# Kernel optimization log

Hardware: AMD Instinct MI355X
Metric: run time of the kernel (lower is better)

The kernel has to match this reference:

```python
import jax, jax.numpy as jnp
import numpy as np

N, D = 8192, 128
WEIGHT = 0.01


def _neg_flat_indices(n):
    # Replicates: mask = ones(n,n); fill_diagonal_(0); mask[i,i+1]=0; mask[i+1,i]=0
    # i.e. keep (i,j) with j != i, j != i+1, j != i-1. Row-major flatnonzero
    # reproduces torch's sim[mask] flattening order exactly.
    i = np.arange(n)[:, None]
    j = np.arange(n)[None, :]
    mask = (j != i) & (j != i + 1) & (j != i - 1)
    idx = np.flatnonzero(mask)
    assert idx.size == (n - 1) * (n - 2)
    return idx


NEG_IDX = jnp.asarray(_neg_flat_indices(N))  # [(N-1)*(N-2)] int32/int64 constant


def setup_inputs() -> dict:
    key = jax.random.key(0)
    factor = jax.random.normal(key, (N, D), dtype=jnp.float32)
    return {"factor": factor}


def reference(factor):
    n = factor.shape[0]
    # F.normalize(factor): L2-normalize rows with eps=1e-12
    norms = jnp.linalg.norm(factor, axis=1, keepdims=True)
    f = factor / jnp.maximum(norms, 1e-12)
    sim = f @ f.T                                   # [N, N] gram matrix
    pos = jnp.diagonal(sim, offset=1).reshape(n - 1, 1)      # [N-1, 1]
    neg = sim.reshape(-1)[NEG_IDX].reshape(n - 1, n - 2)     # [N-1, N-2]
    logits = jnp.concatenate([pos, neg], axis=1)             # [N-1, N-1]
    # CrossEntropyLoss(reduction='sum') with all-zero labels:
    # sum_i (logsumexp(logits_i) - logits_i[0])
    loss = jnp.sum(jax.nn.logsumexp(logits, axis=1) - logits[:, 0])
    loss = loss / n
    return -WEIGHT * loss
```

## Files before the change

### kernel.cpp

```cpp
#include <hip/hip_runtime.h>
#include <hip/hip_bf16.h>

#define N 8192
#define D 128
#define WEIGHT 0.01f
#define NTILES 64
#define NBLK 2080

typedef __bf16 bf16x8 __attribute__((ext_vector_type(8)));
typedef float floatx4 __attribute__((ext_vector_type(4)));

__global__ __launch_bounds__(256) void k_norm(const float* __restrict__ x,
                                              __hip_bfloat16* __restrict__ fb) {
    int gid = blockIdx.x * 256 + threadIdx.x;
    int row = gid >> 4;
    int c   = gid & 15;
    const float4* xr = (const float4*)(x + (size_t)row * D + c * 8);
    float4 f0 = xr[0], f1 = xr[1];
    float s = f0.x * f0.x + f0.y * f0.y + f0.z * f0.z + f0.w * f0.w
            + f1.x * f1.x + f1.y * f1.y + f1.z * f1.z + f1.w * f1.w;
    s += __shfl_xor(s, 1, 64);
    s += __shfl_xor(s, 2, 64);
    s += __shfl_xor(s, 4, 64);
    s += __shfl_xor(s, 8, 64);
    float inv = 1.0f / fmaxf(sqrtf(s), 1e-12f);
    union { __hip_bfloat16 h[8]; uint4 u; } pk;
    pk.h[0] = __float2bfloat16(f0.x * inv);
    pk.h[1] = __float2bfloat16(f0.y * inv);
    pk.h[2] = __float2bfloat16(f0.z * inv);
    pk.h[3] = __float2bfloat16(f0.w * inv);
    pk.h[4] = __float2bfloat16(f1.x * inv);
    pk.h[5] = __float2bfloat16(f1.y * inv);
    pk.h[6] = __float2bfloat16(f1.z * inv);
    pk.h[7] = __float2bfloat16(f1.w * inv);
    ((uint4*)fb)[(size_t)row * 16 + (c ^ (row & 15))] = pk.u;
}

__global__ __launch_bounds__(256, 2) void k_gram(const __hip_bfloat16* __restrict__ fb,
                                                 float* __restrict__ Prow,
                                                 float* __restrict__ Pcol,
                                                 float* __restrict__ p,
                                                 float* __restrict__ ep) {
    int b = blockIdx.x;
    int bi = (int)((2.0 * NTILES + 1.0 - sqrt((2.0 * NTILES + 1.0) * (2.0 * NTILES + 1.0) - 8.0 * (double)b)) * 0.5);
    while (bi * NTILES - bi * (bi - 1) / 2 > b) --bi;
    while ((bi + 1) * NTILES - (bi + 1) * bi / 2 <= b) ++bi;
    int bj = bi + (b - (bi * NTILES - bi * (bi - 1) / 2));

    __shared__ uint4 Ab[128 * 16];
    __shared__ uint4 Bb[128 * 16];
    __shared__ float PR[2][128];
    __shared__ float PC[2][128];

    const int t = threadIdx.x;
    const int lane = t & 63;
    const int wid  = t >> 6;
    const int wrow = wid >> 1, wcol = wid & 1;
    const int col0 = lane & 15;
    const int quad = lane >> 4;
    const int rbase = bi * 128, cbase = bj * 128;

    const uint4* gA = (const uint4*)fb + (size_t)rbase * 16;
    const uint4* gB = (const uint4*)fb + (size_t)cbase * 16;
    #pragma unroll
    for (int i = 0; i < 8; ++i) {
        int ca = wid * 512 + i * 64;
        __builtin_amdgcn_global_load_lds(
            (const __attribute__((address_space(1))) void*)(gA + ca + lane),
            (__attribute__((address_space(3))) void*)&Ab[ca], 16, 0, 0);
        __builtin_amdgcn_global_load_lds(
            (const __attribute__((address_space(1))) void*)(gB + ca + lane),
            (__attribute__((address_space(3))) void*)&Bb[ca], 16, 0, 0);
    }
    __syncthreads();

    floatx4 acc[4][4];
    #pragma unroll
    for (int a = 0; a < 4; ++a)
        #pragma unroll
        for (int c = 0; c < 4; ++c)
            acc[a][c] = (floatx4){0.0f, 0.0f, 0.0f, 0.0f};

    #pragma unroll
    for (int ks = 0; ks < 4; ++ks) {
        bf16x8 af[4], bfr[4];
        int j = ks * 4 + quad;
        int jsw = j ^ col0;
        #pragma unroll
        for (int mt = 0; mt < 4; ++mt) {
            int rl = wrow * 64 + mt * 16 + col0;
            af[mt] = *(const bf16x8*)&Ab[rl * 16 + jsw];
        }
        #pragma unroll
        for (int nt = 0; nt < 4; ++nt) {
            int cl = wcol * 64 + nt * 16 + col0;
            bfr[nt] = *(const bf16x8*)&Bb[cl * 16 + jsw];
        }
        #pragma unroll
        for (int mt = 0; mt < 4; ++mt)
            #pragma unroll
            for (int nt = 0; nt < 4; ++nt)
                acc[mt][nt] = __builtin_amdgcn_mfma_f32_16x16x32_bf16(af[mt], bfr[nt], acc[mt][nt], 0, 0, 0);
    }

    float v[16];
    float colpart[4];
    #pragma unroll
    for (int m = 0; m < 16; ++m) v[m] = 0.0f;
    #pragma unroll
    for (int m = 0; m < 4; ++m) colpart[m] = 0.0f;

    if (bj > bi + 1) {
        #pragma unroll
        for (int mt = 0; mt < 4; ++mt)
            #pragma unroll
            for (int nt = 0; nt < 4; ++nt)
                #pragma unroll
                for (int reg = 0; reg < 4; ++reg) {
                    float e = __expf(acc[mt][nt][reg]);
                    v[mt * 4 + reg] += e;
                    colpart[nt] += e;
                }
    } else {
        #pragma unroll
        for (int mt = 0; mt < 4; ++mt)
            #pragma unroll
            for (int nt = 0; nt < 4; ++nt)
                #pragma unroll
                for (int reg = 0; reg < 4; ++reg) {
                    int r = rbase + wrow * 64 + mt * 16 + quad * 4 + reg;
                    int c = cbase + wcol * 64 + nt * 16 + col0;
                    float s0 = acc[mt][nt][reg];
                    float e = __expf(s0);
                    if (c == r + 1) { p[r] = s0; ep[r] = e; }
                    e = (c > r) ? e : 0.0f;
                    v[mt * 4 + reg] += e;
                    colpart[nt] += e;
                }
    }

    float v8[8];
    #pragma unroll
    for (int k = 0; k < 8; ++k) {
        float a = v[2 * k], bb = v[2 * k + 1];
        float give = (lane & 1) ? a : bb;
        float keep = (lane & 1) ? bb : a;
        v8[k] = keep + __shfl_xor(give, 1, 64);
    }
    float v4[4];
    #pragma unroll
    for (int k = 0; k < 4; ++k) {
        float a = v8[2 * k], bb = v8[2 * k + 1];
        float give = (lane & 2) ? a : bb;
        float keep = (lane & 2) ? bb : a;
        v4[k] = keep + __shfl_xor(give, 2, 64);
    }
    float v2[2];
    #pragma unroll
    for (int k = 0; k < 2; ++k) {
        float a = v4[2 * k], bb = v4[2 * k + 1];
        float give = (lane & 4) ? a : bb;
        float keep = (lane & 4) ? bb : a;
        v2[k] = keep + __shfl_xor(give, 4, 64);
    }
    {
        float a = v2[0], bb = v2[1];
        float give = (lane & 8) ? a : bb;
        float keep = (lane & 8) ? bb : a;
        float v1 = keep + __shfl_xor(give, 8, 64);
        int rowl = wrow * 64 + (col0 >> 2) * 16 + quad * 4 + (col0 & 3);
        PR[wcol][rowl] = v1;
    }
    {
        float c2[2];
        #pragma unroll
        for (int k = 0; k < 2; ++k) {
            float a = colpart[2 * k];
            float bb = colpart[2 * k + 1];
            float give = (lane & 16) ? a : bb;
            float keep = (lane & 16) ? bb : a;
            c2[k] = keep + __shfl_xor(give, 16, 64);
        }
        float a = c2[0], bb = c2[1];
        float give = (lane & 32) ? a : bb;
        float keep = (lane & 32) ? bb : a;
        float cv = keep + __shfl_xor(give, 32, 64);
        PC[wrow][wcol * 64 + lane] = cv;
    }
    __syncthreads();

    if (t < 128) {
        Prow[(size_t)b * 128 + t] = PR[0][t] + PR[1][t];
    } else {
        int c = t - 128;
        Pcol[(size_t)b * 128 + c] = PC[0][c] + PC[1][c];
    }
}

__global__ __launch_bounds__(256) void k_reduce(const float* __restrict__ Prow,
                                                const float* __restrict__ Pcol,
                                                float* __restrict__ U,
                                                float* __restrict__ L) {
    int tile = blockIdx.x;
    int tid = threadIdx.x;
    int base_t = tile * NTILES - tile * (tile - 1) / 2;
    if (tid < 128) {
        float s = 0.0f;
        for (int bj = tile; bj < NTILES; ++bj)
            s += Prow[(size_t)(base_t + bj - tile) * 128 + tid];
        U[tile * 128 + tid] = s;
    } else {
        int c = tid - 128;
        float s = 0.0f;
        for (int bi = 0; bi <= tile; ++bi) {
            int bb = bi * NTILES - bi * (bi - 1) / 2 + (tile - bi);
            s += Pcol[(size_t)bb * 128 + c];
        }
        L[tile * 128 + c] = s;
    }
}

__global__ __launch_bounds__(1024) void k_final(const float* __restrict__ U,
                                                const float* __restrict__ L,
                                                const float* __restrict__ p,
                                                const float* __restrict__ ep,
                                                float* __restrict__ out) {
    __shared__ float swred[16];
    float s = 0.0f;
    for (int i = threadIdx.x; i < N - 1; i += 1024) {
        float tt = U[i] + L[i + 1] - ep[i];
        s += __logf(tt) - p[i];
    }
    #pragma unroll
    for (int m = 1; m < 64; m <<= 1) s += __shfl_xor(s, m, 64);
    int lane = threadIdx.x & 63, wid = threadIdx.x >> 6;
    if (lane == 0) swred[wid] = s;
    __syncthreads();
    if (threadIdx.x == 0) {
        float tot = 0.0f;
        #pragma unroll
        for (int w = 0; w < 16; ++w) tot += swred[w];
        out[0] = -WEIGHT * tot / (float)N;
    }
}

extern "C" void kernel_launch(void* const* d_in, const int* in_sizes, int n_in,
                              void* d_out, int out_size, void* d_ws, size_t ws_size,
                              hipStream_t stream) {
    const float* x = (const float*)d_in[0];
    float* out = (float*)d_out;
    char* ws = (char*)d_ws;
    __hip_bfloat16* fb = (__hip_bfloat16*)ws;
    float* p    = (float*)(ws + (size_t)N * D * 2);
    float* ep   = p + N;
    float* U    = ep + N;
    float* L    = U + N;
    float* Prow = L + N;
    float* Pcol = Prow + (size_t)NBLK * 128;

    hipLaunchKernelGGL(k_norm,   dim3(512),  dim3(256),  0, stream, x, fb);
    hipLaunchKernelGGL(k_gram,   dim3(NBLK), dim3(256),  0, stream, fb, Prow, Pcol, p, ep);
    hipLaunchKernelGGL(k_reduce, dim3(64),   dim3(256),  0, stream, Prow, Pcol, U, L);
    hipLaunchKernelGGL(k_final,  dim3(1),    dim3(1024), 0, stream, U, L, p, ep, out);
}
```

Before: 96.93 us.

## Process four column tiles per block with double-buffered B prefetch

Each k_gram block now handles up to four consecutive column tiles of the same row tile, launching 544 blocks instead of 2080. The A tile is loaded once and reused, while the next B tile is prefetched into a second LDS buffer during the current tile's MFMA and exp work. Partial-sum writeback is deferred by one iteration through double-buffered PR/PC arrays. The intent is to cut redundant A loads and per-block launch and prologue cost. In exchange, launch bounds drop to one block per CU, so occupancy falls and per-row work is uneven because the last chunk of each row has fewer tiles.

```diff
diff --git a/kernel.cpp b/kernel.cpp
--- a/kernel.cpp
+++ b/kernel.cpp
@@ -6,6 +6,8 @@
 #define WEIGHT 0.01f
 #define NTILES 64
 #define NBLK 2080
+#define TPB 4
+#define GRID 544
 
 typedef __bf16 bf16x8 __attribute__((ext_vector_type(8)));
 typedef float floatx4 __attribute__((ext_vector_type(4)));
@@ -36,21 +38,25 @@
     ((uint4*)fb)[(size_t)row * 16 + (c ^ (row & 15))] = pk.u;
 }
 
-__global__ __launch_bounds__(256, 2) void k_gram(const __hip_bfloat16* __restrict__ fb,
+__global__ __launch_bounds__(256, 1) void k_gram(const __hip_bfloat16* __restrict__ fb,
                                                  float* __restrict__ Prow,
                                                  float* __restrict__ Pcol,
                                                  float* __restrict__ p,
                                                  float* __restrict__ ep) {
     int b = blockIdx.x;
-    int bi = (int)((2.0 * NTILES + 1.0 - sqrt((2.0 * NTILES + 1.0) * (2.0 * NTILES + 1.0) - 8.0 * (double)b)) * 0.5);
-    while (bi * NTILES - bi * (bi - 1) / 2 > b) --bi;
-    while ((bi + 1) * NTILES - (bi + 1) * bi / 2 <= b) ++bi;
-    int bj = bi + (b - (bi * NTILES - bi * (bi - 1) / 2));
-
-    __shared__ uint4 Ab[128 * 16];
-    __shared__ uint4 Bb[128 * 16];
-    __shared__ float PR[2][128];
-    __shared__ float PC[2][128];
+    int bi = 0;
+    for (; bi < NTILES; ++bi) {
+        int cnt = (NTILES - bi + TPB - 1) >> 2;
+        if (b < cnt) break;
+        b -= cnt;
+    }
+    int bj0 = bi + b * TPB;
+    int ntile = min(TPB, NTILES - bj0);
+
+    __shared__ uint4 Ab[2048];
+    __shared__ uint4 Bb[2][2048];
+    __shared__ float PR[2][2][128];
+    __shared__ float PC[2][2][128];
 
     const int t = threadIdx.x;
     const int lane = t & 63;
@@ -58,142 +64,181 @@
     const int wrow = wid >> 1, wcol = wid & 1;
     const int col0 = lane & 15;
     const int quad = lane >> 4;
-    const int rbase = bi * 128, cbase = bj * 128;
-
-    const uint4* gA = (const uint4*)fb + (size_t)rbase * 16;
-    const uint4* gB = (const uint4*)fb + (size_t)cbase * 16;
-    #pragma unroll
-    for (int i = 0; i < 8; ++i) {
-        int ca = wid * 512 + i * 64;
-        __builtin_amdgcn_global_load_lds(
-            (const __attribute__((address_space(1))) void*)(gA + ca + lane),
-            (__attribute__((address_space(3))) void*)&Ab[ca], 16, 0, 0);
-        __builtin_amdgcn_global_load_lds(
-            (const __attribute__((address_space(1))) void*)(gB + ca + lane),
-            (__attribute__((address_space(3))) void*)&Bb[ca], 16, 0, 0);
-    }
+    const int rbase = bi * 128;
+    const int tri0 = bi * NTILES - bi * (bi - 1) / 2;
+
+    const uint4* gf = (const uint4*)fb;
+
+    {
+        const uint4* gA = gf + (size_t)rbase * 16;
+        const uint4* gB = gf + (size_t)(bj0 * 128) * 16;
+        #pragma unroll
+        for (int i = 0; i < 8; ++i) {
+            int ca = wid * 512 + i * 64;
+            __builtin_amdgcn_global_load_lds(
+                (const __attribute__((address_space(1))) void*)(gA + ca + lane),
+                (__attribute__((address_space(3))) void*)&Ab[ca], 16, 0, 0);
+            __builtin_amdgcn_global_load_lds(
+                (const __attribute__((address_space(1))) void*)(gB + ca + lane),
+                (__attribute__((address_space(3))) void*)&Bb[0][ca], 16, 0, 0);
+        }
+    }
+
+    for (int tt = 0; tt < ntile; ++tt) {
+        const int cur = tt & 1;
+        const int bjt = bj0 + tt;
+        const int cbase = bjt * 128;
+        const int tgid = tri0 + (bjt - bi);
+
+        __syncthreads();
+
+        if (tt + 1 < ntile) {
+            const uint4* gBn = gf + (size_t)((bjt + 1) * 128) * 16;
+            #pragma unroll
+            for (int i = 0; i < 8; ++i) {
+                int ca = wid * 512 + i * 64;
+                __builtin_amdgcn_global_load_lds(
+                    (const __attribute__((address_space(1))) void*)(gBn + ca + lane),
+                    (__attribute__((address_space(3))) void*)&Bb[cur ^ 1][ca], 16, 0, 0);
+            }
+        }
+
+        if (tt > 0) {
+            int pprev = (tt - 1) & 1;
+            int tprev = tgid - 1;
+            if (t < 128) {
+                Prow[(size_t)tprev * 128 + t] = PR[pprev][0][t] + PR[pprev][1][t];
+            } else {
+                int c = t - 128;
+                Pcol[(size_t)tprev * 128 + c] = PC[pprev][0][c] + PC[pprev][1][c];
+            }
+        }
+
+        floatx4 acc[4][4];
+        #pragma unroll
+        for (int a = 0; a < 4; ++a)
+            #pragma unroll
+            for (int c = 0; c < 4; ++c)
+                acc[a][c] = (floatx4){0.0f, 0.0f, 0.0f, 0.0f};
+
+        #pragma unroll
+        for (int ks = 0; ks < 4; ++ks) {
+            bf16x8 af[4], bfr[4];
+            int j = ks * 4 + quad;
+            int jsw = j ^ col0;
+            #pragma unroll
+            for (int mt = 0; mt < 4; ++mt) {
+                int rl = wrow * 64 + mt * 16 + col0;
+                af[mt] = *(const bf16x8*)&Ab[rl * 16 + jsw];
+            }
+            #pragma unroll
+            for (int nt = 0; nt < 4; ++nt) {
+                int cl = wcol * 64 + nt * 16 + col0;
+                bfr[nt] = *(const bf16x8*)&Bb[cur][cl * 16 + jsw];
+            }
+            #pragma unroll
+            for (int mt = 0; mt < 4; ++mt)
+                #pragma unroll
+                for (int nt = 0; nt < 4; ++nt)
+                    acc[mt][nt] = __builtin_amdgcn_mfma_f32_16x16x32_bf16(af[mt], bfr[nt], acc[mt][nt], 0, 0, 0);
+        }
+
+        float v[16];
+        float colpart[4];
+        #pragma unroll
+        for (int m = 0; m < 16; ++m) v[m] = 0.0f;
+        #pragma unroll
+        for (int m = 0; m < 4; ++m) colpart[m] = 0.0f;
+
+        if (bjt > bi + 1) {
+            #pragma unroll
+            for (int mt = 0; mt < 4; ++mt)
+                #pragma unroll
+                for (int nt = 0; nt < 4; ++nt)
+                    #pragma unroll
+                    for (int reg = 0; reg < 4; ++reg) {
+                        float e = __expf(acc[mt][nt][reg]);
+                        v[mt * 4 + reg] += e;
+                        colpart[nt] += e;
+                    }
+        } else {
+            #pragma unroll
+            for (int mt = 0; mt < 4; ++mt)
+                #pragma unroll
+                for (int nt = 0; nt < 4; ++nt)
+                    #pragma unroll
+                    for (int reg = 0; reg < 4; ++reg) {
+                        int r = rbase + wrow * 64 + mt * 16 + quad * 4 + reg;
+                        int c = cbase + wcol * 64 + nt * 16 + col0;
+                        float s0 = acc[mt][nt][reg];
+                        float e = __expf(s0);
+                        if (c == r + 1) { p[r] = s0; ep[r] = e; }
+                        e = (c > r) ? e : 0.0f;
+                        v[mt * 4 + reg] += e;
+                        colpart[nt] += e;
+                    }
+        }
+
+        float v8[8];
+        #pragma unroll
+        for (int k = 0; k < 8; ++k) {
+            float a = v[2 * k], bb = v[2 * k + 1];
+            float give = (lane & 1) ? a : bb;
+            float keep = (lane & 1) ? bb : a;
+            v8[k] = keep + __shfl_xor(give, 1, 64);
+        }
+        float v4[4];
+        #pragma unroll
+        for (int k = 0; k < 4; ++k) {
+            float a = v8[2 * k], bb = v8[2 * k + 1];
+            float give = (lane & 2) ? a : bb;
+            float keep = (lane & 2) ? bb : a;
+            v4[k] = keep + __shfl_xor(give, 2, 64);
+        }
+        float v2[2];
+        #pragma unroll
+        for (int k = 0; k < 2; ++k) {
+            float a = v4[2 * k], bb = v4[2 * k + 1];
+            float give = (lane & 4) ? a : bb;
+            float keep = (lane & 4) ? bb : a;
+            v2[k] = keep + __shfl_xor(give, 4, 64);
+        }
+        {
+            float a = v2[0], bb = v2[1];
+            float give = (lane & 8) ? a : bb;
+            float keep = (lane & 8) ? bb : a;
+            float v1 = keep + __shfl_xor(give, 8, 64);
+            int rowl = wrow * 64 + (col0 >> 2) * 16 + quad * 4 + (col0 & 3);
+            PR[cur][wcol][rowl] = v1;
+        }
+        {
+            float c2[2];
+            #pragma unroll
+            for (int k = 0; k < 2; ++k) {
+                float a = colpart[2 * k];
+                float bb = colpart[2 * k + 1];
+                float give = (lane & 16) ? a : bb;
+                float keep = (lane & 16) ? bb : a;
+                c2[k] = keep + __shfl_xor(give, 16, 64);
+            }
+            float a = c2[0], bb = c2[1];
+            float give = (lane & 32) ? a : bb;
+            float keep = (lane & 32) ? bb : a;
+            float cv = keep + __shfl_xor(give, 32, 64);
+            PC[cur][wrow][wcol * 64 + lane] = cv;
+        }
+    }
+
     __syncthreads();
-
-    floatx4 acc[4][4];
-    #pragma unroll
-    for (int a = 0; a < 4; ++a)
-        #pragma unroll
-        for (int c = 0; c < 4; ++c)
-            acc[a][c] = (floatx4){0.0f, 0.0f, 0.0f, 0.0f};
-
-    #pragma unroll
-    for (int ks = 0; ks < 4; ++ks) {
-        bf16x8 af[4], bfr[4];
-        int j = ks * 4 + quad;
-        int jsw = j ^ col0;
-        #pragma unroll
-        for (int mt = 0; mt < 4; ++mt) {
-            int rl = wrow * 64 + mt * 16 + col0;
-            af[mt] = *(const bf16x8*)&Ab[rl * 16 + jsw];
-        }
-        #pragma unroll
-        for (int nt = 0; nt < 4; ++nt) {
-            int cl = wcol * 64 + nt * 16 + col0;
-            bfr[nt] = *(const bf16x8*)&Bb[cl * 16 + jsw];
-        }
-        #pragma unroll
-        for (int mt = 0; mt < 4; ++mt)
-            #pragma unroll
-            for (int nt = 0; nt < 4; ++nt)
-                acc[mt][nt] = __builtin_amdgcn_mfma_f32_16x16x32_bf16(af[mt], bfr[nt], acc[mt][nt], 0, 0, 0);
-    }
-
-    float v[16];
-    float colpart[4];
-    #pragma unroll
-    for (int m = 0; m < 16; ++m) v[m] = 0.0f;
-    #pragma unroll
-    for (int m = 0; m < 4; ++m) colpart[m] = 0.0f;
-
-    if (bj > bi + 1) {
-        #pragma unroll
-        for (int mt = 0; mt < 4; ++mt)
-            #pragma unroll
-            for (int nt = 0; nt < 4; ++nt)
-                #pragma unroll
-                for (int reg = 0; reg < 4; ++reg) {
-                    float e = __expf(acc[mt][nt][reg]);
-                    v[mt * 4 + reg] += e;
-                    colpart[nt] += e;
-                }
-    } else {
-        #pragma unroll
-        for (int mt = 0; mt < 4; ++mt)
-            #pragma unroll
-            for (int nt = 0; nt < 4; ++nt)
-                #pragma unroll
-                for (int reg = 0; reg < 4; ++reg) {
-                    int r = rbase + wrow * 64 + mt * 16 + quad * 4 + reg;
-                    int c = cbase + wcol * 64 + nt * 16 + col0;
-                    float s0 = acc[mt][nt][reg];
-                    float e = __expf(s0);
-                    if (c == r + 1) { p[r] = s0; ep[r] = e; }
-                    e = (c > r) ? e : 0.0f;
-                    v[mt * 4 + reg] += e;
-                    colpart[nt] += e;
-                }
-    }
-
-    float v8[8];
-    #pragma unroll
-    for (int k = 0; k < 8; ++k) {
-        float a = v[2 * k], bb = v[2 * k + 1];
-        float give = (lane & 1) ? a : bb;
-        float keep = (lane & 1) ? bb : a;
-        v8[k] = keep + __shfl_xor(give, 1, 64);
-    }
-    float v4[4];
-    #pragma unroll
-    for (int k = 0; k < 4; ++k) {
-        float a = v8[2 * k], bb = v8[2 * k + 1];
-        float give = (lane & 2) ? a : bb;
-        float keep = (lane & 2) ? bb : a;
-        v4[k] = keep + __shfl_xor(give, 2, 64);
-    }
-    float v2[2];
-    #pragma unroll
-    for (int k = 0; k < 2; ++k) {
-        float a = v4[2 * k], bb = v4[2 * k + 1];
-        float give = (lane & 4) ? a : bb;
-        float keep = (lane & 4) ? bb : a;
-        v2[k] = keep + __shfl_xor(give, 4, 64);
-    }
     {
-        float a = v2[0], bb = v2[1];
-        float give = (lane & 8) ? a : bb;
-        float keep = (lane & 8) ? bb : a;
-        float v1 = keep + __shfl_xor(give, 8, 64);
-        int rowl = wrow * 64 + (col0 >> 2) * 16 + quad * 4 + (col0 & 3);
-        PR[wcol][rowl] = v1;
-    }
-    {
-        float c2[2];
-        #pragma unroll
-        for (int k = 0; k < 2; ++k) {
-            float a = colpart[2 * k];
-            float bb = colpart[2 * k + 1];
-            float give = (lane & 16) ? a : bb;
-            float keep = (lane & 16) ? bb : a;
-            c2[k] = keep + __shfl_xor(give, 16, 64);
-        }
-        float a = c2[0], bb = c2[1];
-        float give = (lane & 32) ? a : bb;
-        float keep = (lane & 32) ? bb : a;
-        float cv = keep + __shfl_xor(give, 32, 64);
-        PC[wrow][wcol * 64 + lane] = cv;
-    }
-    __syncthreads();
-
-    if (t < 128) {
-        Prow[(size_t)b * 128 + t] = PR[0][t] + PR[1][t];
-    } else {
-        int c = t - 128;
-        Pcol[(size_t)b * 128 + c] = PC[0][c] + PC[1][c];
+        int pprev = (ntile - 1) & 1;
+        int tprev = tri0 + (bj0 + ntile - 1 - bi);
+        if (t < 128) {
+            Prow[(size_t)tprev * 128 + t] = PR[pprev][0][t] + PR[pprev][1][t];
+        } else {
+            int c = t - 128;
+            Pcol[(size_t)tprev * 128 + c] = PC[pprev][0][c] + PC[pprev][1][c];
+        }
     }
 }
 
@@ -259,7 +304,7 @@
     float* Pcol = Prow + (size_t)NBLK * 128;
 
     hipLaunchKernelGGL(k_norm,   dim3(512),  dim3(256),  0, stream, x, fb);
-    hipLaunchKernelGGL(k_gram,   dim3(NBLK), dim3(256),  0, stream, fb, Prow, Pcol, p, ep);
+    hipLaunchKernelGGL(k_gram,   dim3(GRID), dim3(256),  0, stream, fb, Prow, Pcol, p, ep);
     hipLaunchKernelGGL(k_reduce, dim3(64),   dim3(256),  0, stream, Prow, Pcol, U, L);
     hipLaunchKernelGGL(k_final,  dim3(1),    dim3(1024), 0, stream, U, L, p, ep, out);
 }
```

Result: slower. 109.2 us (+12.6%).

## Enlarge gram tiles to 256x256 with 512-thread blocks

Applied to the files above, without the earlier changes.

Doubles the upper-triangle gram tile from 128 to 256 rows and columns and uses 8 waves per block, each wave computing a 64x128 output slab. This cuts the block count from 2080 to 528, halves the per-element partial-sum traffic, and shrinks the reduction kernel to 32 tiles. The aim is better reuse of each loaded operand and less partial-sum writing and reduction overhead. In exchange, LDS use rises to about 128KB per block, which likely limits occupancy to one block per CU. The much smaller grid also risks poor load balance across CUs.

```diff
diff --git a/kernel.cpp b/kernel.cpp
--- a/kernel.cpp
+++ b/kernel.cpp
@@ -4,8 +4,8 @@
 #define N 8192
 #define D 128
 #define WEIGHT 0.01f
-#define NTILES 64
-#define NBLK 2080
+#define NT2 32
+#define NBLK2 528
 
 typedef __bf16 bf16x8 __attribute__((ext_vector_type(8)));
 typedef float floatx4 __attribute__((ext_vector_type(4)));
@@ -36,29 +36,28 @@
     ((uint4*)fb)[(size_t)row * 16 + (c ^ (row & 15))] = pk.u;
 }
 
-__global__ __launch_bounds__(256, 2) void k_gram(const __hip_bfloat16* __restrict__ fb,
+__global__ __launch_bounds__(512, 2) void k_gram(const __hip_bfloat16* __restrict__ fb,
                                                  float* __restrict__ Prow,
                                                  float* __restrict__ Pcol,
                                                  float* __restrict__ p,
                                                  float* __restrict__ ep) {
     int b = blockIdx.x;
-    int bi = (int)((2.0 * NTILES + 1.0 - sqrt((2.0 * NTILES + 1.0) * (2.0 * NTILES + 1.0) - 8.0 * (double)b)) * 0.5);
-    while (bi * NTILES - bi * (bi - 1) / 2 > b) --bi;
-    while ((bi + 1) * NTILES - (bi + 1) * bi / 2 <= b) ++bi;
-    int bj = bi + (b - (bi * NTILES - bi * (bi - 1) / 2));
-
-    __shared__ uint4 Ab[128 * 16];
-    __shared__ uint4 Bb[128 * 16];
-    __shared__ float PR[2][128];
-    __shared__ float PC[2][128];
+    int bi = 0;
+    while ((bi + 1) * NT2 - (bi + 1) * bi / 2 <= b) ++bi;
+    int bj = bi + (b - (bi * NT2 - bi * (bi - 1) / 2));
+
+    __shared__ uint4 Ab[4096];
+    __shared__ uint4 Bb[4096];
+    __shared__ float PR[2][256];
+    __shared__ float PC[4][256];
 
     const int t = threadIdx.x;
     const int lane = t & 63;
     const int wid  = t >> 6;
-    const int wrow = wid >> 1, wcol = wid & 1;
+    const int wrow = wid & 3, wcol = wid >> 2;
     const int col0 = lane & 15;
     const int quad = lane >> 4;
-    const int rbase = bi * 128, cbase = bj * 128;
+    const int rbase = bi * 256, cbase = bj * 256;
 
     const uint4* gA = (const uint4*)fb + (size_t)rbase * 16;
     const uint4* gB = (const uint4*)fb + (size_t)cbase * 16;
@@ -74,16 +73,16 @@
     }
     __syncthreads();
 
-    floatx4 acc[4][4];
+    floatx4 acc[4][8];
     #pragma unroll
     for (int a = 0; a < 4; ++a)
         #pragma unroll
-        for (int c = 0; c < 4; ++c)
+        for (int c = 0; c < 8; ++c)
             acc[a][c] = (floatx4){0.0f, 0.0f, 0.0f, 0.0f};
 
     #pragma unroll
     for (int ks = 0; ks < 4; ++ks) {
-        bf16x8 af[4], bfr[4];
+        bf16x8 af[4], bfr[8];
         int j = ks * 4 + quad;
         int jsw = j ^ col0;
         #pragma unroll
@@ -92,29 +91,29 @@
             af[mt] = *(const bf16x8*)&Ab[rl * 16 + jsw];
         }
         #pragma unroll
-        for (int nt = 0; nt < 4; ++nt) {
-            int cl = wcol * 64 + nt * 16 + col0;
+        for (int nt = 0; nt < 8; ++nt) {
+            int cl = wcol * 128 + nt * 16 + col0;
             bfr[nt] = *(const bf16x8*)&Bb[cl * 16 + jsw];
         }
         #pragma unroll
         for (int mt = 0; mt < 4; ++mt)
             #pragma unroll
-            for (int nt = 0; nt < 4; ++nt)
+            for (int nt = 0; nt < 8; ++nt)
                 acc[mt][nt] = __builtin_amdgcn_mfma_f32_16x16x32_bf16(af[mt], bfr[nt], acc[mt][nt], 0, 0, 0);
     }
 
     float v[16];
-    float colpart[4];
+    float colpart[8];
     #pragma unroll
     for (int m = 0; m < 16; ++m) v[m] = 0.0f;
     #pragma unroll
-    for (int m = 0; m < 4; ++m) colpart[m] = 0.0f;
+    for (int m = 0; m < 8; ++m) colpart[m] = 0.0f;
 
     if (bj > bi + 1) {
         #pragma unroll
         for (int mt = 0; mt < 4; ++mt)
             #pragma unroll
-            for (int nt = 0; nt < 4; ++nt)
+            for (int nt = 0; nt < 8; ++nt)
                 #pragma unroll
                 for (int reg = 0; reg < 4; ++reg) {
                     float e = __expf(acc[mt][nt][reg]);
@@ -125,11 +124,11 @@
         #pragma unroll
         for (int mt = 0; mt < 4; ++mt)
             #pragma unroll
-            for (int nt = 0; nt < 4; ++nt)
+            for (int nt = 0; nt < 8; ++nt)
                 #pragma unroll
                 for (int reg = 0; reg < 4; ++reg) {
                     int r = rbase + wrow * 64 + mt * 16 + quad * 4 + reg;
-                    int c = cbase + wcol * 64 + nt * 16 + col0;
+                    int c = cbase + wcol * 128 + nt * 16 + col0;
                     float s0 = acc[mt][nt][reg];
                     float e = __expf(s0);
                     if (c == r + 1) { p[r] = s0; ep[r] = e; }
@@ -172,51 +171,54 @@
         PR[wcol][rowl] = v1;
     }
     {
-        float c2[2];
-        #pragma unroll
-        for (int k = 0; k < 2; ++k) {
+        float c4[4];
+        #pragma unroll
+        for (int k = 0; k < 4; ++k) {
             float a = colpart[2 * k];
             float bb = colpart[2 * k + 1];
             float give = (lane & 16) ? a : bb;
             float keep = (lane & 16) ? bb : a;
-            c2[k] = keep + __shfl_xor(give, 16, 64);
-        }
-        float a = c2[0], bb = c2[1];
-        float give = (lane & 32) ? a : bb;
-        float keep = (lane & 32) ? bb : a;
-        float cv = keep + __shfl_xor(give, 32, 64);
-        PC[wrow][wcol * 64 + lane] = cv;
+            c4[k] = keep + __shfl_xor(give, 16, 64);
+        }
+        #pragma unroll
+        for (int k = 0; k < 2; ++k) {
+            float a = c4[2 * k], bb = c4[2 * k + 1];
+            float give = (lane & 32) ? a : bb;
+            float keep = (lane & 32) ? bb : a;
+            float cv = keep + __shfl_xor(give, 32, 64);
+            PC[wrow][wcol * 128 + k * 64 + lane] = cv;
+        }
     }
     __syncthreads();
 
-    if (t < 128) {
-        Prow[(size_t)b * 128 + t] = PR[0][t] + PR[1][t];
+    if (t < 256) {
+        Prow[(size_t)blockIdx.x * 256 + t] = PR[0][t] + PR[1][t];
     } else {
-        int c = t - 128;
-        Pcol[(size_t)b * 128 + c] = PC[0][c] + PC[1][c];
-    }
-}
-
-__global__ __launch_bounds__(256) void k_reduce(const float* __restrict__ Prow,
+        int c = t - 256;
+        Pcol[(size_t)blockIdx.x * 256 + c] = PC[0][c] + PC[1][c] + PC[2][c] + PC[3][c];
+    }
+}
+
+__global__ __launch_bounds__(512) void k_reduce(const float* __restrict__ Prow,
                                                 const float* __restrict__ Pcol,
                                                 float* __restrict__ U,
                                                 float* __restrict__ L) {
     int tile = blockIdx.x;
     int tid = threadIdx.x;
-    int base_t = tile * NTILES - tile * (tile - 1) / 2;
-    if (tid < 128) {
+    int base_t = tile * NT2 - tile * (tile - 1) / 2;
+    if (tid < 256) {
         float s = 0.0f;
-        for (int bj = tile; bj < NTILES; ++bj)
-            s += Prow[(size_t)(base_t + bj - tile) * 128 + tid];
-        U[tile * 128 + tid] = s;
+        for (int bj = tile; bj < NT2; ++bj)
+            s += Prow[(size_t)(base_t + bj - tile) * 256 + tid];
+        U[tile * 256 + tid] = s;
     } else {
-        int c = tid - 128;
+        int c = tid - 256;
         float s = 0.0f;
         for (int bi = 0; bi <= tile; ++bi) {
-            int bb = bi * NTILES - bi * (bi - 1) / 2 + (tile - bi);
-            s += Pcol[(size_t)bb * 128 + c];
-        }
-        L[tile * 128 + c] = s;
+            int bb = bi * NT2 - bi * (bi - 1) / 2 + (tile - bi);
+            s += Pcol[(size_t)bb * 256 + c];
+        }
+        L[tile * 256 + c] = s;
     }
 }
 
@@ -256,10 +258,10 @@
     float* U    = ep + N;
     float* L    = U + N;
     float* Prow = L + N;
-    float* Pcol = Prow + (size_t)NBLK * 128;
-
-    hipLaunchKernelGGL(k_norm,   dim3(512),  dim3(256),  0, stream, x, fb);
-    hipLaunchKernelGGL(k_gram,   dim3(NBLK), dim3(256),  0, stream, fb, Prow, Pcol, p, ep);
-    hipLaunchKernelGGL(k_reduce, dim3(64),   dim3(256),  0, stream, Prow, Pcol, U, L);
-    hipLaunchKernelGGL(k_final,  dim3(1),    dim3(1024), 0, stream, U, L, p, ep, out);
-}
+    float* Pcol = Prow + (size_t)NBLK2 * 256;
+
+    hipLaunchKernelGGL(k_norm,   dim3(512),   dim3(256),  0, stream, x, fb);
+    hipLaunchKernelGGL(k_gram,   dim3(NBLK2), dim3(512),  0, stream, fb, Prow, Pcol, p, ep);
+    hipLaunchKernelGGL(k_reduce, dim3(32),    dim3(512),  0, stream, Prow, Pcol, U, L);
+    hipLaunchKernelGGL(k_final,  dim3(1),     dim3(1024), 0, stream, U, L, p, ep, out);
+}
```

Result: no change. 97.98 us (+1.1%).

## Fuse gram, reduce and final into persistent kernel with grid barrier

Applied to the files above, without the earlier changes.

Replaces the three launches (gram over 2080 tiles, per-tile reduce, single-block final) with one persistent kernel of 256 blocks. Each block loops over tiles, then waits at a spin-wait grid barrier built on an atomic counter. After the barrier, every block reduces 32 rows of partials, takes the logs, and adds its partial sum into an atomic accumulator; the last block to arrive writes the output. The aim is to cut launch overhead and the serial tail of the old single-block final kernel. In exchange, the tile loop serializes work within each block, each tile costs an extra barrier, and the spin barrier depends on all 256 blocks being resident at once.

```diff
diff --git a/kernel.cpp b/kernel.cpp
--- a/kernel.cpp
+++ b/kernel.cpp
@@ -6,13 +6,18 @@
 #define WEIGHT 0.01f
 #define NTILES 64
 #define NBLK 2080
+#define PBLK 256
 
 typedef __bf16 bf16x8 __attribute__((ext_vector_type(8)));
 typedef float floatx4 __attribute__((ext_vector_type(4)));
 
 __global__ __launch_bounds__(256) void k_norm(const float* __restrict__ x,
-                                              __hip_bfloat16* __restrict__ fb) {
+                                              __hip_bfloat16* __restrict__ fb,
+                                              float* __restrict__ acc,
+                                              unsigned* __restrict__ done,
+                                              unsigned* __restrict__ cnt2) {
     int gid = blockIdx.x * 256 + threadIdx.x;
+    if (gid == 0) { *acc = 0.0f; *done = 0u; *cnt2 = 0u; }
     int row = gid >> 4;
     int c   = gid & 15;
     const float4* xr = (const float4*)(x + (size_t)row * D + c * 8);
@@ -36,21 +41,20 @@
     ((uint4*)fb)[(size_t)row * 16 + (c ^ (row & 15))] = pk.u;
 }
 
-__global__ __launch_bounds__(256, 2) void k_gram(const __hip_bfloat16* __restrict__ fb,
+__global__ __launch_bounds__(256, 2) void k_main(const __hip_bfloat16* __restrict__ fb,
                                                  float* __restrict__ Prow,
                                                  float* __restrict__ Pcol,
                                                  float* __restrict__ p,
-                                                 float* __restrict__ ep) {
-    int b = blockIdx.x;
-    int bi = (int)((2.0 * NTILES + 1.0 - sqrt((2.0 * NTILES + 1.0) * (2.0 * NTILES + 1.0) - 8.0 * (double)b)) * 0.5);
-    while (bi * NTILES - bi * (bi - 1) / 2 > b) --bi;
-    while ((bi + 1) * NTILES - (bi + 1) * bi / 2 <= b) ++bi;
-    int bj = bi + (b - (bi * NTILES - bi * (bi - 1) / 2));
-
-    __shared__ uint4 Ab[128 * 16];
-    __shared__ uint4 Bb[128 * 16];
+                                                 float* __restrict__ ep,
+                                                 float* __restrict__ acc,
+                                                 unsigned* __restrict__ done,
+                                                 unsigned* __restrict__ cnt2,
+                                                 float* __restrict__ out) {
+    __shared__ uint4 Ab[2048];
+    __shared__ uint4 Bb[2048];
     __shared__ float PR[2][128];
     __shared__ float PC[2][128];
+    __shared__ float swred[4];
 
     const int t = threadIdx.x;
     const int lane = t & 63;
@@ -58,189 +62,194 @@
     const int wrow = wid >> 1, wcol = wid & 1;
     const int col0 = lane & 15;
     const int quad = lane >> 4;
-    const int rbase = bi * 128, cbase = bj * 128;
-
-    const uint4* gA = (const uint4*)fb + (size_t)rbase * 16;
-    const uint4* gB = (const uint4*)fb + (size_t)cbase * 16;
-    #pragma unroll
-    for (int i = 0; i < 8; ++i) {
-        int ca = wid * 512 + i * 64;
-        __builtin_amdgcn_global_load_lds(
-            (const __attribute__((address_space(1))) void*)(gA + ca + lane),
-            (__attribute__((address_space(3))) void*)&Ab[ca], 16, 0, 0);
-        __builtin_amdgcn_global_load_lds(
-            (const __attribute__((address_space(1))) void*)(gB + ca + lane),
-            (__attribute__((address_space(3))) void*)&Bb[ca], 16, 0, 0);
+    const uint4* gf = (const uint4*)fb;
+
+    for (int tile = blockIdx.x; tile < NBLK; tile += PBLK) {
+        int bi = 0;
+        while ((bi + 1) * NTILES - (bi + 1) * bi / 2 <= tile) ++bi;
+        int bj = bi + (tile - (bi * NTILES - bi * (bi - 1) / 2));
+        const int rbase = bi * 128, cbase = bj * 128;
+
+        const uint4* gA = gf + (size_t)rbase * 16;
+        const uint4* gB = gf + (size_t)cbase * 16;
+        #pragma unroll
+        for (int i = 0; i < 8; ++i) {
+            int ca = wid * 512 + i * 64;
+            __builtin_amdgcn_global_load_lds(
+                (const __attribute__((address_space(1))) void*)(gA + ca + lane),
+                (__attribute__((address_space(3))) void*)&Ab[ca], 16, 0, 0);
+            __builtin_amdgcn_global_load_lds(
+                (const __attribute__((address_space(1))) void*)(gB + ca + lane),
+                (__attribute__((address_space(3))) void*)&Bb[ca], 16, 0, 0);
+        }
+        __syncthreads();
+
+        floatx4 acc4[4][4];
+        #pragma unroll
+        for (int a = 0; a < 4; ++a)
+            #pragma unroll
+            for (int c = 0; c < 4; ++c)
+                acc4[a][c] = (floatx4){0.0f, 0.0f, 0.0f, 0.0f};
+
+        #pragma unroll
+        for (int ks = 0; ks < 4; ++ks) {
+            bf16x8 af[4], bfr[4];
+            int j = ks * 4 + quad;
+            int jsw = j ^ col0;
+            #pragma unroll
+            for (int mt = 0; mt < 4; ++mt) {
+                int rl = wrow * 64 + mt * 16 + col0;
+                af[mt] = *(const bf16x8*)&Ab[rl * 16 + jsw];
+            }
+            #pragma unroll
+            for (int nt = 0; nt < 4; ++nt) {
+                int cl = wcol * 64 + nt * 16 + col0;
+                bfr[nt] = *(const bf16x8*)&Bb[cl * 16 + jsw];
+            }
+            #pragma unroll
+            for (int mt = 0; mt < 4; ++mt)
+                #pragma unroll
+                for (int nt = 0; nt < 4; ++nt)
+                    acc4[mt][nt] = __builtin_amdgcn_mfma_f32_16x16x32_bf16(af[mt], bfr[nt], acc4[mt][nt], 0, 0, 0);
+        }
+
+        float v[16];
+        float colpart[4];
+        #pragma unroll
+        for (int m = 0; m < 16; ++m) v[m] = 0.0f;
+        #pragma unroll
+        for (int m = 0; m < 4; ++m) colpart[m] = 0.0f;
+
+        if (bj > bi + 1) {
+            #pragma unroll
+            for (int mt = 0; mt < 4; ++mt)
+                #pragma unroll
+                for (int nt = 0; nt < 4; ++nt)
+                    #pragma unroll
+                    for (int reg = 0; reg < 4; ++reg) {
+                        float e = __expf(acc4[mt][nt][reg]);
+                        v[mt * 4 + reg] += e;
+                        colpart[nt] += e;
+                    }
+        } else {
+            #pragma unroll
+            for (int mt = 0; mt < 4; ++mt)
+                #pragma unroll
+                for (int nt = 0; nt < 4; ++nt)
+                    #pragma unroll
+                    for (int reg = 0; reg < 4; ++reg) {
+                        int r = rbase + wrow * 64 + mt * 16 + quad * 4 + reg;
+                        int c = cbase + wcol * 64 + nt * 16 + col0;
+                        float s0 = acc4[mt][nt][reg];
+                        float e = __expf(s0);
+                        if (c == r + 1) { p[r] = s0; ep[r] = e; }
+                        e = (c > r) ? e : 0.0f;
+                        v[mt * 4 + reg] += e;
+                        colpart[nt] += e;
+                    }
+        }
+
+        float v8[8];
+        #pragma unroll
+        for (int k = 0; k < 8; ++k) {
+            float a = v[2 * k], bb = v[2 * k + 1];
+            float give = (lane & 1) ? a : bb;
+            float keep = (lane & 1) ? bb : a;
+            v8[k] = keep + __shfl_xor(give, 1, 64);
+        }
+        float v4[4];
+        #pragma unroll
+        for (int k = 0; k < 4; ++k) {
+            float a = v8[2 * k], bb = v8[2 * k + 1];
+            float give = (lane & 2) ? a : bb;
+            float keep = (lane & 2) ? bb : a;
+            v4[k] = keep + __shfl_xor(give, 2, 64);
+        }
+        float v2[2];
+        #pragma unroll
+        for (int k = 0; k < 2; ++k) {
+            float a = v4[2 * k], bb = v4[2 * k + 1];
+            float give = (lane & 4) ? a : bb;
+            float keep = (lane & 4) ? bb : a;
+            v2[k] = keep + __shfl_xor(give, 4, 64);
+        }
+        {
+            float a = v2[0], bb = v2[1];
+            float give = (lane & 8) ? a : bb;
+            float keep = (lane & 8) ? bb : a;
+            float v1 = keep + __shfl_xor(give, 8, 64);
+            int rowl = wrow * 64 + (col0 >> 2) * 16 + quad * 4 + (col0 & 3);
+            PR[wcol][rowl] = v1;
+        }
+        {
+            float c2[2];
+            #pragma unroll
+            for (int k = 0; k < 2; ++k) {
+                float a = colpart[2 * k];
+                float bb = colpart[2 * k + 1];
+                float give = (lane & 16) ? a : bb;
+                float keep = (lane & 16) ? bb : a;
+                c2[k] = keep + __shfl_xor(give, 16, 64);
+            }
+            float a = c2[0], bb = c2[1];
+            float give = (lane & 32) ? a : bb;
+            float keep = (lane & 32) ? bb : a;
+            float cv = keep + __shfl_xor(give, 32, 64);
+            PC[wrow][wcol * 64 + lane] = cv;
+        }
+        __syncthreads();
+
+        if (t < 128) {
+            Prow[(size_t)tile * 128 + t] = PR[0][t] + PR[1][t];
+        } else {
+            int c = t - 128;
+            Pcol[(size_t)tile * 128 + c] = PC[0][c] + PC[1][c];
+        }
+        __syncthreads();
+    }
+
+    __threadfence();
+    __syncthreads();
+    if (t == 0) {
+        __hip_atomic_fetch_add(done, 1u, __ATOMIC_RELEASE, __HIP_MEMORY_SCOPE_AGENT);
+        while (__hip_atomic_load(done, __ATOMIC_ACQUIRE, __HIP_MEMORY_SCOPE_AGENT) < PBLK)
+            __builtin_amdgcn_s_sleep(8);
     }
     __syncthreads();
 
-    floatx4 acc[4][4];
-    #pragma unroll
-    for (int a = 0; a < 4; ++a)
-        #pragma unroll
-        for (int c = 0; c < 4; ++c)
-            acc[a][c] = (floatx4){0.0f, 0.0f, 0.0f, 0.0f};
-
-    #pragma unroll
-    for (int ks = 0; ks < 4; ++ks) {
-        bf16x8 af[4], bfr[4];
-        int j = ks * 4 + quad;
-        int jsw = j ^ col0;
-        #pragma unroll
-        for (int mt = 0; mt < 4; ++mt) {
-            int rl = wrow * 64 + mt * 16 + col0;
-            af[mt] = *(const bf16x8*)&Ab[rl * 16 + jsw];
-        }
-        #pragma unroll
-        for (int nt = 0; nt < 4; ++nt) {
-            int cl = wcol * 64 + nt * 16 + col0;
-            bfr[nt] = *(const bf16x8*)&Bb[cl * 16 + jsw];
-        }
-        #pragma unroll
-        for (int mt = 0; mt < 4; ++mt)
-            #pragma unroll
-            for (int nt = 0; nt < 4; ++nt)
-                acc[mt][nt] = __builtin_amdgcn_mfma_f32_16x16x32_bf16(af[mt], bfr[nt], acc[mt][nt], 0, 0, 0);
-    }
-
-    float v[16];
-    float colpart[4];
-    #pragma unroll
-    for (int m = 0; m < 16; ++m) v[m] = 0.0f;
-    #pragma unroll
-    for (int m = 0; m < 4; ++m) colpart[m] = 0.0f;
-
-    if (bj > bi + 1) {
-        #pragma unroll
-        for (int mt = 0; mt < 4; ++mt)
-            #pragma unroll
-            for (int nt = 0; nt < 4; ++nt)
-                #pragma unroll
-                for (int reg = 0; reg < 4; ++reg) {
-                    float e = __expf(acc[mt][nt][reg]);
-                    v[mt * 4 + reg] += e;
-                    colpart[nt] += e;
-                }
-    } else {
-        #pragma unroll
-        for (int mt = 0; mt < 4; ++mt)
-            #pragma unroll
-            for (int nt = 0; nt < 4; ++nt)
-                #pragma unroll
-                for (int reg = 0; reg < 4; ++reg) {
-                    int r = rbase + wrow * 64 + mt * 16 + quad * 4 + reg;
-                    int c = cbase + wcol * 64 + nt * 16 + col0;
-                    float s0 = acc[mt][nt][reg];
-                    float e = __expf(s0);
-                    if (c == r + 1) { p[r] = s0; ep[r] = e; }
-                    e = (c > r) ? e : 0.0f;
-                    v[mt * 4 + reg] += e;
-                    colpart[nt] += e;
-                }
-    }
-
-    float v8[8];
-    #pragma unroll
-    for (int k = 0; k < 8; ++k) {
-        float a = v[2 * k], bb = v[2 * k + 1];
-        float give = (lane & 1) ? a : bb;
-        float keep = (lane & 1) ? bb : a;
-        v8[k] = keep + __shfl_xor(give, 1, 64);
-    }
-    float v4[4];
-    #pragma unroll
-    for (int k = 0; k < 4; ++k) {
-        float a = v8[2 * k], bb = v8[2 * k + 1];
-        float give = (lane & 2) ? a : bb;
-        float keep = (lane & 2) ? bb : a;
-        v4[k] = keep + __shfl_xor(give, 2, 64);
-    }
-    float v2[2];
-    #pragma unroll
-    for (int k = 0; k < 2; ++k) {
-        float a = v4[2 * k], bb = v4[2 * k + 1];
-        float give = (lane & 4) ? a : bb;
-        float keep = (lane & 4) ? bb : a;
-        v2[k] = keep + __shfl_xor(give, 4, 64);
-    }
     {
-        float a = v2[0], bb = v2[1];
-        float give = (lane & 8) ? a : bb;
-        float keep = (lane & 8) ? bb : a;
-        float v1 = keep + __shfl_xor(give, 8, 64);
-        int rowl = wrow * 64 + (col0 >> 2) * 16 + quad * 4 + (col0 & 3);
-        PR[wcol][rowl] = v1;
-    }
-    {
-        float c2[2];
-        #pragma unroll
-        for (int k = 0; k < 2; ++k) {
-            float a = colpart[2 * k];
-            float bb = colpart[2 * k + 1];
-            float give = (lane & 16) ? a : bb;
-            float keep = (lane & 16) ? bb : a;
-            c2[k] = keep + __shfl_xor(give, 16, 64);
-        }
-        float a = c2[0], bb = c2[1];
-        float give = (lane & 32) ? a : bb;
-        float keep = (lane & 32) ? bb : a;
-        float cv = keep + __shfl_xor(give, 32, 64);
-        PC[wrow][wcol * 64 + lane] = cv;
-    }
-    __syncthreads();
-
-    if (t < 128) {
-        Prow[(size_t)b * 128 + t] = PR[0][t] + PR[1][t];
-    } else {
-        int c = t - 128;
-        Pcol[(size_t)b * 128 + c] = PC[0][c] + PC[1][c];
-    }
-}
-
-__global__ __launch_bounds__(256) void k_reduce(const float* __restrict__ Prow,
-                                                const float* __restrict__ Pcol,
-                                                float* __restrict__ U,
-                                                float* __restrict__ L) {
-    int tile = blockIdx.x;
-    int tid = threadIdx.x;
-    int base_t = tile * NTILES - tile * (tile - 1) / 2;
-    if (tid < 128) {
+        int r = blockIdx.x * 32 + (t >> 3);
+        int tsub = t & 7;
         float s = 0.0f;
-        for (int bj = tile; bj < NTILES; ++bj)
-            s += Prow[(size_t)(base_t + bj - tile) * 128 + tid];
-        U[tile * 128 + tid] = s;
-    } else {
-        int c = tid - 128;
-        float s = 0.0f;
-        for (int bi = 0; bi <= tile; ++bi) {
-            int bb = bi * NTILES - bi * (bi - 1) / 2 + (tile - bi);
-            s += Pcol[(size_t)bb * 128 + c];
-        }
-        L[tile * 128 + c] = s;
-    }
-}
-
-__global__ __launch_bounds__(1024) void k_final(const float* __restrict__ U,
-                                                const float* __restrict__ L,
-                                                const float* __restrict__ p,
-                                                const float* __restrict__ ep,
-                                                float* __restrict__ out) {
-    __shared__ float swred[16];
-    float s = 0.0f;
-    for (int i = threadIdx.x; i < N - 1; i += 1024) {
-        float tt = U[i] + L[i + 1] - ep[i];
-        s += __logf(tt) - p[i];
-    }
-    #pragma unroll
-    for (int m = 1; m < 64; m <<= 1) s += __shfl_xor(s, m, 64);
-    int lane = threadIdx.x & 63, wid = threadIdx.x >> 6;
-    if (lane == 0) swred[wid] = s;
-    __syncthreads();
-    if (threadIdx.x == 0) {
-        float tot = 0.0f;
-        #pragma unroll
-        for (int w = 0; w < 16; ++w) tot += swred[w];
-        out[0] = -WEIGHT * tot / (float)N;
+        int band = r >> 7;
+        int baseU = band * NTILES - band * (band - 1) / 2;
+        for (int bj = band + tsub; bj < NTILES; bj += 8)
+            s += Prow[(size_t)(baseU + bj - band) * 128 + (r & 127)];
+        if (r < N - 1) {
+            int c = r + 1;
+            int bandc = c >> 7;
+            for (int bi = tsub; bi <= bandc; bi += 8)
+                s += Pcol[(size_t)(bi * NTILES - bi * (bi - 1) / 2 + (bandc - bi)) * 128 + (c & 127)];
+        }
+        s += __shfl_xor(s, 1, 64);
+        s += __shfl_xor(s, 2, 64);
+        s += __shfl_xor(s, 4, 64);
+        float term = 0.0f;
+        if (tsub == 0 && r < N - 1)
+            term = __logf(s - ep[r]) - p[r];
+        #pragma unroll
+        for (int m = 8; m < 64; m <<= 1) term += __shfl_xor(term, m, 64);
+        if (lane == 0) swred[wid] = term;
+        __syncthreads();
+        if (t == 0) {
+            float part = swred[0] + swred[1] + swred[2] + swred[3];
+            __hip_atomic_fetch_add(acc, part, __ATOMIC_RELEASE, __HIP_MEMORY_SCOPE_AGENT);
+            unsigned old = __hip_atomic_fetch_add(cnt2, 1u, __ATOMIC_ACQ_REL, __HIP_MEMORY_SCOPE_AGENT);
+            if (old == PBLK - 1) {
+                float tot = __hip_atomic_load(acc, __ATOMIC_ACQUIRE, __HIP_MEMORY_SCOPE_AGENT);
+                out[0] = -WEIGHT * tot / (float)N;
+            }
+        }
     }
 }
 
@@ -253,13 +262,13 @@
     __hip_bfloat16* fb = (__hip_bfloat16*)ws;
     float* p    = (float*)(ws + (size_t)N * D * 2);
     float* ep   = p + N;
-    float* U    = ep + N;
-    float* L    = U + N;
-    float* Prow = L + N;
+    float* Prow = ep + N;
     float* Pcol = Prow + (size_t)NBLK * 128;
-
-    hipLaunchKernelGGL(k_norm,   dim3(512),  dim3(256),  0, stream, x, fb);
-    hipLaunchKernelGGL(k_gram,   dim3(NBLK), dim3(256),  0, stream, fb, Prow, Pcol, p, ep);
-    hipLaunchKernelGGL(k_reduce, dim3(64),   dim3(256),  0, stream, Prow, Pcol, U, L);
-    hipLaunchKernelGGL(k_final,  dim3(1),    dim3(1024), 0, stream, U, L, p, ep, out);
+    float* acc  = Pcol + (size_t)NBLK * 128;
+    unsigned* done = (unsigned*)(acc + 1);
+    unsigned* cnt2 = done + 1;
+
+    hipLaunchKernelGGL(k_norm, dim3(512),  dim3(256), 0, stream, x, fb, acc, done, cnt2);
+    hipLaunchKernelGGL(k_main, dim3(PBLK), dim3(256), 0, stream, fb, Prow, Pcol, p, ep,
+                       acc, done, cnt2, out);
 }
```

Measured after the change: 129.7 us. 33.8% more time.
